# Performance work log

Measured on AMD Instinct MI355X. Metric: run time of the kernel, lower is better.

Reference implementation:

```python
import jax, jax.numpy as jnp
import numpy as np

B, L, H, S = 8, 2048, 8, 128


def setup_inputs() -> dict:
    key = jax.random.key(0)
    k1, k2, k3 = jax.random.split(key, 3)
    x = jax.random.normal(k1, (B, L, S), dtype=jnp.float32)
    W = jax.random.normal(k2, (L, H), dtype=jnp.float32)          # per-head Toeplitz logits, W[j, h] fills diagonal -j
    A = jax.random.normal(k3, (H * S, H * S), dtype=jnp.float32)  # bilinear form for stage-2 attention
    return {"x": x, "W": W, "A": A}


def reference(x, W, A):
    Bb, Ll, Ss = x.shape
    Hh = W.shape[1]
    HS = Hh * Ss
    # Stage 1: causal Toeplitz softmax attention per head.
    # Original fills diagonal -j of W_h with W[j, h], masks strictly-upper with -inf, softmaxes rows.
    d = jnp.arange(Ll)[:, None] - jnp.arange(Ll)[None, :]          # (L, L), i - j
    logits = jnp.where(d[..., None] >= 0,
                       W[jnp.clip(d, 0, Ll - 1)],                  # (L, L, H), W[i-j, h] on valid band
                       -jnp.inf)
    P = jax.nn.softmax(logits, axis=1)                             # softmax over key axis j
    attn = jnp.einsum('ijh,bjs->bihs', P, x).reshape(Bb, Ll, HS)   # heads concatenated
    X1 = jnp.concatenate([attn, x], axis=-1)                       # (B, L, (H+1)*S)
    # Stage 2: single-query bilinear attention from last token over previous tokens.
    q = X1[:, -1, :HS]                                             # (B, HS)
    keys = X1[:, :-1, :HS]                                         # (B, L-1, HS)
    scores = jnp.einsum('bd,de,ble->bl', q, A, keys)               # (B, L-1)
    w2 = jax.nn.softmax(scores, axis=-1)
    # values are the raw-x slice X1[:, :-1, HS:] == x[:, :-1, :]
    out = jnp.einsum('bl,bls->bs', w2, x[:, :-1, :])               # (B, S)
    return out
```

## Files before the change

### kernel.cpp

```cpp
#include <hip/hip_runtime.h>

#define L 2048
#define H 8
#define S 128
#define B 8
#define HS 1024

__global__ __launch_bounds__(512) void kA_prep_qpart(const float* __restrict__ W,
                                                     const float* __restrict__ x,
                                                     float* __restrict__ Eb,
                                                     float* __restrict__ Zb,
                                                     float* __restrict__ partial_q,
                                                     unsigned* __restrict__ counters) {
  const int b = blockIdx.x, jc = blockIdx.y;
  const int t = threadIdx.x;
  if (b == 0 && jc == 0 && t == 0) counters[0] = 0u;

  __shared__ float ew[128][H];
  __shared__ float part[16][H][S];
  __shared__ float tot[512];

  const int base = jc * 128;
  const int dhi = L - 1 - base;
#pragma unroll
  for (int k = 0; k < 2; ++k) {
    const int idx = t + k * 512;
    const int i = idx >> 3, h = idx & 7;
    ew[i][h] = expf(W[(size_t)(dhi - i) * H + h]);
  }

  if (jc < H) {
    const int h = jc;
    const int d0 = t * 4;
    float e[4];
    float run = 0.f;
#pragma unroll
    for (int k = 0; k < 4; ++k) {
      float v = expf(W[(size_t)(d0 + k) * H + h]);
      e[k] = v; run += v;
    }
    tot[t] = run;
    __syncthreads();
    for (int off = 1; off < 512; off <<= 1) {
      float v = (t >= off) ? tot[t - off] : 0.f;
      __syncthreads();
      tot[t] += v;
      __syncthreads();
    }
    float c = (t == 0) ? 0.f : tot[t - 1];
    const size_t ebase = (size_t)(b * H + h) * L;
#pragma unroll
    for (int k = 0; k < 4; ++k) {
      c += e[k];
      Eb[ebase + d0 + k] = e[k];
      Zb[ebase + d0 + k] = c;
    }
  }
  __syncthreads();

  const int s4 = t & 31;
  const int r = t >> 5;
  const float4* __restrict__ x4 = (const float4*)(x + (size_t)b * L * S);
  float4 acc[H];
#pragma unroll
  for (int h = 0; h < H; ++h) acc[h] = make_float4(0.f, 0.f, 0.f, 0.f);
#pragma unroll
  for (int k = 0; k < 8; ++k) {
    const int ll = k * 16 + r;
    const int l = base + ll;
    const float4 xv = x4[(size_t)l * 32 + s4];
#pragma unroll
    for (int h = 0; h < H; ++h) {
      const float w = ew[ll][h];
      acc[h].x += w * xv.x; acc[h].y += w * xv.y;
      acc[h].z += w * xv.z; acc[h].w += w * xv.w;
    }
  }
#pragma unroll
  for (int h = 0; h < H; ++h) {
    part[r][h][s4 * 4 + 0] = acc[h].x;
    part[r][h][s4 * 4 + 1] = acc[h].y;
    part[r][h][s4 * 4 + 2] = acc[h].z;
    part[r][h][s4 * 4 + 3] = acc[h].w;
  }
  __syncthreads();
#pragma unroll
  for (int k = 0; k < 2; ++k) {
    const int idx = t + k * 512;
    const int h = idx >> 7, s = idx & 127;
    float sm = 0.f;
#pragma unroll
    for (int rr = 0; rr < 16; ++rr) sm += part[rr][h][s];
    partial_q[((size_t)b * 16 + jc) * HS + idx] = sm;
  }
}

__global__ __launch_bounds__(512) void kB_v(const float* __restrict__ partial_q,
                                            const float* __restrict__ Zb,
                                            const float* __restrict__ A,
                                            float* __restrict__ partial_v) {
  const int ebase = blockIdx.x * 128;
  const int dc = blockIdx.y;
  const int dbase = dc * 64;
  const int t = threadIdx.x;
  __shared__ float ql[8][64];
  __shared__ float p2[4][8][128];
  const float invZ = 1.f / Zb[(size_t)(dc >> 1) * L + (L - 1)];
  {
    const int bb = t >> 6, dl = t & 63;
    const float* __restrict__ pq = partial_q + ((size_t)bb * 16) * HS + dbase + dl;
    float a0 = 0.f, a1 = 0.f, a2 = 0.f, a3 = 0.f;
#pragma unroll
    for (int j4 = 0; j4 < 16; j4 += 4) {
      a0 += pq[(size_t)(j4 + 0) * HS];
      a1 += pq[(size_t)(j4 + 1) * HS];
      a2 += pq[(size_t)(j4 + 2) * HS];
      a3 += pq[(size_t)(j4 + 3) * HS];
    }
    ql[bb][dl] = ((a0 + a1) + (a2 + a3)) * invZ;
  }
  __syncthreads();
  const int el = t & 127, dg = t >> 7;
  const int e = ebase + el;
  const float* __restrict__ Ab = A + (size_t)(dbase + dg * 16) * HS + e;
  float acc[8] = {0.f, 0.f, 0.f, 0.f, 0.f, 0.f, 0.f, 0.f};
#pragma unroll 4
  for (int dd = 0; dd < 16; ++dd) {
    const float a = Ab[(size_t)dd * HS];
    const int d = dg * 16 + dd;
    acc[0] += ql[0][d] * a;
    acc[1] += ql[1][d] * a;
    acc[2] += ql[2][d] * a;
    acc[3] += ql[3][d] * a;
    acc[4] += ql[4][d] * a;
    acc[5] += ql[5][d] * a;
    acc[6] += ql[6][d] * a;
    acc[7] += ql[7][d] * a;
  }
#pragma unroll
  for (int bb = 0; bb < 8; ++bb) p2[dg][bb][el] = acc[bb];
  __syncthreads();
#pragma unroll
  for (int k = 0; k < 2; ++k) {
    const int idx = t + k * 512;
    const int bb = idx >> 7, el2 = idx & 127;
    partial_v[((size_t)bb * 16 + dc) * HS + ebase + el2] =
        (p2[0][bb][el2] + p2[1][bb][el2]) + (p2[2][bb][el2] + p2[3][bb][el2]);
  }
}

__global__ __launch_bounds__(512) void kC_u(const float* __restrict__ x,
                                            const float* __restrict__ partial_v,
                                            float* __restrict__ u_pad) {
  const int b = blockIdx.x, jc = blockIdx.y;
  const int t = threadIdx.x;
  __shared__ float vs[HS];
  __shared__ float up[4][H][128];
#pragma unroll
  for (int k = 0; k < 2; ++k) {
    const int i = t + k * 512;
    float a0 = 0.f, a1 = 0.f, a2 = 0.f, a3 = 0.f;
#pragma unroll
    for (int dcc = 0; dcc < 16; dcc += 4) {
      a0 += partial_v[((size_t)b * 16 + dcc + 0) * HS + i];
      a1 += partial_v[((size_t)b * 16 + dcc + 1) * HS + i];
      a2 += partial_v[((size_t)b * 16 + dcc + 2) * HS + i];
      a3 += partial_v[((size_t)b * 16 + dcc + 3) * HS + i];
    }
    vs[i] = (a0 + a1) + (a2 + a3);
  }
  __syncthreads();
  const int jl = t & 127, sq = t >> 7;
  const int j = jc * 128 + jl;
  const float4* __restrict__ xr = (const float4*)(x + ((size_t)b * L + j) * S) + sq * 8;
  float4 xv[8];
#pragma unroll
  for (int i = 0; i < 8; ++i) xv[i] = xr[i];
  float acc[H];
#pragma unroll
  for (int h = 0; h < H; ++h) {
    const float4* __restrict__ vv = (const float4*)(vs + h * S + sq * 32);
    float a = 0.f;
#pragma unroll
    for (int i = 0; i < 8; ++i) {
      const float4 w = vv[i];
      a += xv[i].x * w.x + xv[i].y * w.y + xv[i].z * w.z + xv[i].w * w.w;
    }
    acc[h] = a;
  }
#pragma unroll
  for (int h = 0; h < H; ++h) up[sq][h][jl] = acc[h];
  __syncthreads();
#pragma unroll
  for (int k = 0; k < 2; ++k) {
    const int idx = t + k * 512;
    const int h = idx >> 7, j2 = idx & 127;
    const float sv = (up[0][h][j2] + up[1][h][j2]) + (up[2][h][j2] + up[3][h][j2]);
    const size_t rowbase = (size_t)(b * H + h) * (2 * L);
    u_pad[rowbase + jc * 128 + j2] = 0.f;
    u_pad[rowbase + L + jc * 128 + j2] = sv;
  }
}

__global__ __launch_bounds__(512) void kD_conv(const float* __restrict__ u_pad,
                                               const float* __restrict__ Eb,
                                               const float* __restrict__ Zb,
                                               float* __restrict__ partial_s) {
  const int b = blockIdx.x;
  const int rr = blockIdx.y;
  int lt = 0, c = 0;
  while (c + (lt / 2 + 1) <= rr) { c += lt / 2 + 1; ++lt; }
  const int dtt = rr - c;
  const int l0 = lt * 128;
  const int t = threadIdx.x;
  const int tsub = t & 31;
  const int h = (t >> 5) & 7;
  const int dh = t >> 8;
  const int dbase = dtt * 256 + dh * 128;
  const int Lb = l0 + tsub * 4;
  const float* __restrict__ ur = u_pad + (size_t)(b * H + h) * (2 * L) + L;
  const float4* __restrict__ Eh4 = (const float4*)(Eb + (size_t)(b * H + h) * L);
  float acc0 = 0.f, acc1 = 0.f, acc2 = 0.f, acc3 = 0.f;
  float4 lo = *(const float4*)(ur + Lb - dbase - 4);
  float4 hi = *(const float4*)(ur + Lb - dbase);
#pragma unroll 4
  for (int dd = 0; dd < 128; dd += 4) {
    const int d0 = dbase + dd;
    float4 ev  = Eh4[d0 >> 2];
    float4 nlo = *(const float4*)(ur + Lb - d0 - 8);
    acc0 += ev.x * hi.x; acc1 += ev.x * hi.y; acc2 += ev.x * hi.z; acc3 += ev.x * hi.w;
    acc0 += ev.y * lo.w; acc1 += ev.y * hi.x; acc2 += ev.y * hi.y; acc3 += ev.y * hi.z;
    acc0 += ev.z * lo.z; acc1 += ev.z * lo.w; acc2 += ev.z * hi.x; acc3 += ev.z * hi.y;
    acc0 += ev.w * lo.y; acc1 += ev.w * lo.z; acc2 += ev.w * lo.w; acc3 += ev.w * hi.x;
    hi = lo; lo = nlo;
  }
  __shared__ float sred[2][H][128];
  const float4 zv = *(const float4*)&Zb[(size_t)(b * H + h) * L + Lb];
  sred[dh][h][tsub * 4 + 0] = acc0 / zv.x;
  sred[dh][h][tsub * 4 + 1] = acc1 / zv.y;
  sred[dh][h][tsub * 4 + 2] = acc2 / zv.z;
  sred[dh][h][tsub * 4 + 3] = acc3 / zv.w;
  __syncthreads();
  if (t < 128) {
    float sc = 0.f;
#pragma unroll
    for (int hh = 0; hh < H; ++hh) sc += sred[0][hh][t] + sred[1][hh][t];
    partial_s[((size_t)b * 8 + dtt) * L + l0 + t] = sc;
  }
}

__global__ __launch_bounds__(512) void kF_out(const float* __restrict__ x,
                                              const float* __restrict__ partial_s,
                                              float* __restrict__ partial,
                                              unsigned* __restrict__ counters,
                                              float* __restrict__ out) {
  const int b = blockIdx.x, c = blockIdx.y;
  const int t = threadIdx.x;
  __shared__ float ep[L];
  __shared__ float red[512];
  __shared__ float part[16][S];

  const int l0 = t * 4;
  const int ltq = t >> 6;
  float sc[4] = {0.f, 0.f, 0.f, 0.f};
  for (int dtt = 0; dtt <= ltq; ++dtt) {
    const float4 a = *(const float4*)(partial_s + ((size_t)b * 8 + dtt) * L + l0);
    sc[0] += a.x; sc[1] += a.y; sc[2] += a.z; sc[3] += a.w;
  }
  if (t == 511) sc[3] = -3.4e38f;
  float mx = fmaxf(fmaxf(sc[0], sc[1]), fmaxf(sc[2], sc[3]));
  red[t] = mx;
  __syncthreads();
  for (int off = 256; off > 0; off >>= 1) {
    if (t < off) red[t] = fmaxf(red[t], red[t + off]);
    __syncthreads();
  }
  mx = red[0];
  __syncthreads();
  float e[4];
  float sm = 0.f;
#pragma unroll
  for (int k = 0; k < 4; ++k) {
    e[k] = (l0 + k < L - 1) ? expf(sc[k] - mx) : 0.f;
    sm += e[k];
  }
  red[t] = sm;
  __syncthreads();
  for (int off = 256; off > 0; off >>= 1) {
    if (t < off) red[t] += red[t + off];
    __syncthreads();
  }
  const float inv = 1.f / red[0];
#pragma unroll
  for (int k = 0; k < 4; ++k) ep[l0 + k] = e[k] * inv;
  __syncthreads();

  const int s4 = t & 31;
  const int r = t >> 5;
  const int base = c * 128;
  const float4* __restrict__ x4 = (const float4*)(x + (size_t)b * L * S);
  float4 acc = make_float4(0.f, 0.f, 0.f, 0.f);
#pragma unroll
  for (int k = 0; k < 8; ++k) {
    const int l = base + k * 16 + r;
    const float w = ep[l];
    const float4 xv = x4[(size_t)l * 32 + s4];
    acc.x += w * xv.x; acc.y += w * xv.y; acc.z += w * xv.z; acc.w += w * xv.w;
  }
  part[r][s4 * 4 + 0] = acc.x;
  part[r][s4 * 4 + 1] = acc.y;
  part[r][s4 * 4 + 2] = acc.z;
  part[r][s4 * 4 + 3] = acc.w;
  __syncthreads();
  if (t < S) {
    float smv = 0.f;
#pragma unroll
    for (int rr = 0; rr < 16; ++rr) smv += part[rr][t];
    partial[((size_t)b * 16 + c) * S + t] = smv;
  }
  __threadfence();
  __syncthreads();
  __shared__ unsigned lastFlag;
  if (t == 0)
    lastFlag = (atomicAdd(&counters[0], 1u) == (unsigned)(B * 16 - 1)) ? 1u : 0u;
  __syncthreads();
  if (lastFlag) {
#pragma unroll
    for (int k = 0; k < 2; ++k) {
      const int idx = t + k * 512;
      const int b2 = idx >> 7, s = idx & 127;
      float a = 0.f;
#pragma unroll 4
      for (int cc = 0; cc < 16; ++cc) a += partial[((size_t)b2 * 16 + cc) * S + s];
      out[b2 * S + s] = a;
    }
  }
}

extern "C" void kernel_launch(void* const* d_in, const int* in_sizes, int n_in,
                              void* d_out, int out_size, void* d_ws, size_t ws_size,
                              hipStream_t stream) {
  const float* x = (const float*)d_in[0];
  const float* W = (const float*)d_in[1];
  const float* A = (const float*)d_in[2];
  float* out = (float*)d_out;

  float* ws        = (float*)d_ws;
  float* Eb        = ws;
  float* Zb        = Eb + (size_t)B * H * L;
  float* partial_q = Zb + (size_t)B * H * L;
  float* partial_v = partial_q + (size_t)B * 16 * HS;
  float* u_pad     = partial_v + (size_t)B * 16 * HS;
  float* partial_s = u_pad + (size_t)B * H * 2 * L;
  float* partial   = partial_s + (size_t)B * 8 * L;
  unsigned* counters = (unsigned*)(partial + (size_t)B * 16 * S);

  kA_prep_qpart<<<dim3(B, 16), 512, 0, stream>>>(W, x, Eb, Zb, partial_q, counters);
  kB_v         <<<dim3(8, 16), 512, 0, stream>>>(partial_q, Zb, A, partial_v);
  kC_u         <<<dim3(B, 16), 512, 0, stream>>>(x, partial_v, u_pad);
  kD_conv      <<<dim3(B, 72), 512, 0, stream>>>(u_pad, Eb, Zb, partial_s);
  kF_out       <<<dim3(B, 16), 512, 0, stream>>>(x, partial_s, partial, counters, out);
}
```

Before: 55.93 us.

## Fuse convolution and output kernels with per-batch last-block softmax reduction

Merges the convolution kernel and the softmax/output kernel into one launch. Each block now loops over all causal diagonal chunks for its row tile instead of splitting chunks across 72 blocks per batch, and writes full scores directly. The last block per batch, found with a per-batch atomic counter, does the softmax and the full weighted sum over x. This removes a kernel launch and the partial-score buffer, but drops parallelism: the grid shrinks from 72 to 16 blocks per batch with uneven per-block work, and one block per batch does the whole output reduction serially.

Result: slower. 62.76 us (+12.2%).

```diff
diff --git a/kernel.cpp b/kernel.cpp
--- a/kernel.cpp
+++ b/kernel.cpp
@@ -14,7 +14,7 @@
                                                      unsigned* __restrict__ counters) {
   const int b = blockIdx.x, jc = blockIdx.y;
   const int t = threadIdx.x;
-  if (b == 0 && jc == 0 && t == 0) counters[0] = 0u;
+  if (b == 0 && jc == 0 && t < 8) counters[t] = 0u;
 
   __shared__ float ew[128][H];
   __shared__ float part[16][H][S];
@@ -202,39 +202,45 @@
   }
 }
 
-__global__ __launch_bounds__(512) void kD_conv(const float* __restrict__ u_pad,
+__global__ __launch_bounds__(512) void kDF_out(const float* __restrict__ x,
+                                               const float* __restrict__ u_pad,
                                                const float* __restrict__ Eb,
                                                const float* __restrict__ Zb,
-                                               float* __restrict__ partial_s) {
-  const int b = blockIdx.x;
-  const int rr = blockIdx.y;
-  int lt = 0, c = 0;
-  while (c + (lt / 2 + 1) <= rr) { c += lt / 2 + 1; ++lt; }
-  const int dtt = rr - c;
-  const int l0 = lt * 128;
+                                               float* __restrict__ scores,
+                                               unsigned* __restrict__ counters,
+                                               float* __restrict__ out) {
+  const int b = blockIdx.x, lt = blockIdx.y;
   const int t = threadIdx.x;
   const int tsub = t & 31;
   const int h = (t >> 5) & 7;
   const int dh = t >> 8;
-  const int dbase = dtt * 256 + dh * 128;
+  const int l0 = lt * 128;
   const int Lb = l0 + tsub * 4;
+
+  __shared__ float sred[2][H][128];
+  __shared__ float ep[L];
+  __shared__ float red[512];
+  __shared__ float part[16][S];
+
   const float* __restrict__ ur = u_pad + (size_t)(b * H + h) * (2 * L) + L;
   const float4* __restrict__ Eh4 = (const float4*)(Eb + (size_t)(b * H + h) * L);
   float acc0 = 0.f, acc1 = 0.f, acc2 = 0.f, acc3 = 0.f;
-  float4 lo = *(const float4*)(ur + Lb - dbase - 4);
-  float4 hi = *(const float4*)(ur + Lb - dbase);
+  for (int chunk = dh; chunk <= lt; chunk += 2) {
+    const int dbase = chunk * 128;
+    float4 lo = *(const float4*)(ur + Lb - dbase - 4);
+    float4 hi = *(const float4*)(ur + Lb - dbase);
 #pragma unroll 4
-  for (int dd = 0; dd < 128; dd += 4) {
-    const int d0 = dbase + dd;
-    float4 ev  = Eh4[d0 >> 2];
-    float4 nlo = *(const float4*)(ur + Lb - d0 - 8);
-    acc0 += ev.x * hi.x; acc1 += ev.x * hi.y; acc2 += ev.x * hi.z; acc3 += ev.x * hi.w;
-    acc0 += ev.y * lo.w; acc1 += ev.y * hi.x; acc2 += ev.y * hi.y; acc3 += ev.y * hi.z;
-    acc0 += ev.z * lo.z; acc1 += ev.z * lo.w; acc2 += ev.z * hi.x; acc3 += ev.z * hi.y;
-    acc0 += ev.w * lo.y; acc1 += ev.w * lo.z; acc2 += ev.w * lo.w; acc3 += ev.w * hi.x;
-    hi = lo; lo = nlo;
-  }
-  __shared__ float sred[2][H][128];
+    for (int dd = 0; dd < 128; dd += 4) {
+      const int d0 = dbase + dd;
+      float4 ev  = Eh4[d0 >> 2];
+      float4 nlo = *(const float4*)(ur + Lb - d0 - 8);
+      acc0 += ev.x * hi.x; acc1 += ev.x * hi.y; acc2 += ev.x * hi.z; acc3 += ev.x * hi.w;
+      acc0 += ev.y * lo.w; acc1 += ev.y * hi.x; acc2 += ev.y * hi.y; acc3 += ev.y * hi.z;
+      acc0 += ev.z * lo.z; acc1 += ev.z * lo.w; acc2 += ev.z * hi.x; acc3 += ev.z * hi.y;
+      acc0 += ev.w * lo.y; acc1 += ev.w * lo.z; acc2 += ev.w * lo.w; acc3 += ev.w * hi.x;
+      hi = lo; lo = nlo;
+    }
+  }
   const float4 zv = *(const float4*)&Zb[(size_t)(b * H + h) * L + Lb];
   sred[dh][h][tsub * 4 + 0] = acc0 / zv.x;
   sred[dh][h][tsub * 4 + 1] = acc1 / zv.y;
@@ -242,33 +248,24 @@
   sred[dh][h][tsub * 4 + 3] = acc3 / zv.w;
   __syncthreads();
   if (t < 128) {
+    const int l = l0 + t;
     float sc = 0.f;
 #pragma unroll
     for (int hh = 0; hh < H; ++hh) sc += sred[0][hh][t] + sred[1][hh][t];
-    partial_s[((size_t)b * 8 + dtt) * L + l0 + t] = sc;
-  }
-}
-
-__global__ __launch_bounds__(512) void kF_out(const float* __restrict__ x,
-                                              const float* __restrict__ partial_s,
-                                              float* __restrict__ partial,
-                                              unsigned* __restrict__ counters,
-                                              float* __restrict__ out) {
-  const int b = blockIdx.x, c = blockIdx.y;
-  const int t = threadIdx.x;
-  __shared__ float ep[L];
-  __shared__ float red[512];
-  __shared__ float part[16][S];
-
-  const int l0 = t * 4;
-  const int ltq = t >> 6;
-  float sc[4] = {0.f, 0.f, 0.f, 0.f};
-  for (int dtt = 0; dtt <= ltq; ++dtt) {
-    const float4 a = *(const float4*)(partial_s + ((size_t)b * 8 + dtt) * L + l0);
-    sc[0] += a.x; sc[1] += a.y; sc[2] += a.z; sc[3] += a.w;
-  }
-  if (t == 511) sc[3] = -3.4e38f;
-  float mx = fmaxf(fmaxf(sc[0], sc[1]), fmaxf(sc[2], sc[3]));
+    scores[(size_t)b * L + l] = (l == L - 1) ? -3.4e38f : sc;
+  }
+
+  __threadfence();
+  __syncthreads();
+  __shared__ unsigned lastFlag;
+  if (t == 0)
+    lastFlag = (atomicAdd(&counters[b], 1u) == 15u) ? 1u : 0u;
+  __syncthreads();
+  if (!lastFlag) return;
+
+  const int l4 = t * 4;
+  const float4 sv4 = *(const float4*)&scores[(size_t)b * L + l4];
+  float mx = fmaxf(fmaxf(sv4.x, sv4.y), fmaxf(sv4.z, sv4.w));
   red[t] = mx;
   __syncthreads();
   for (int off = 256; off > 0; off >>= 1) {
@@ -277,32 +274,27 @@
   }
   mx = red[0];
   __syncthreads();
-  float e[4];
-  float sm = 0.f;
-#pragma unroll
-  for (int k = 0; k < 4; ++k) {
-    e[k] = (l0 + k < L - 1) ? expf(sc[k] - mx) : 0.f;
-    sm += e[k];
-  }
-  red[t] = sm;
+  float e0 = expf(sv4.x - mx), e1 = expf(sv4.y - mx);
+  float e2 = expf(sv4.z - mx), e3 = expf(sv4.w - mx);
+  red[t] = (e0 + e1) + (e2 + e3);
   __syncthreads();
   for (int off = 256; off > 0; off >>= 1) {
     if (t < off) red[t] += red[t + off];
     __syncthreads();
   }
   const float inv = 1.f / red[0];
-#pragma unroll
-  for (int k = 0; k < 4; ++k) ep[l0 + k] = e[k] * inv;
+  ep[l4 + 0] = e0 * inv;
+  ep[l4 + 1] = e1 * inv;
+  ep[l4 + 2] = e2 * inv;
+  ep[l4 + 3] = e3 * inv;
   __syncthreads();
 
   const int s4 = t & 31;
   const int r = t >> 5;
-  const int base = c * 128;
   const float4* __restrict__ x4 = (const float4*)(x + (size_t)b * L * S);
   float4 acc = make_float4(0.f, 0.f, 0.f, 0.f);
-#pragma unroll
-  for (int k = 0; k < 8; ++k) {
-    const int l = base + k * 16 + r;
+  for (int k = 0; k < 128; ++k) {
+    const int l = k * 16 + r;
     const float w = ep[l];
     const float4 xv = x4[(size_t)l * 32 + s4];
     acc.x += w * xv.x; acc.y += w * xv.y; acc.z += w * xv.z; acc.w += w * xv.w;
@@ -316,24 +308,7 @@
     float smv = 0.f;
 #pragma unroll
     for (int rr = 0; rr < 16; ++rr) smv += part[rr][t];
-    partial[((size_t)b * 16 + c) * S + t] = smv;
-  }
-  __threadfence();
-  __syncthreads();
-  __shared__ unsigned lastFlag;
-  if (t == 0)
-    lastFlag = (atomicAdd(&counters[0], 1u) == (unsigned)(B * 16 - 1)) ? 1u : 0u;
-  __syncthreads();
-  if (lastFlag) {
-#pragma unroll
-    for (int k = 0; k < 2; ++k) {
-      const int idx = t + k * 512;
-      const int b2 = idx >> 7, s = idx & 127;
-      float a = 0.f;
-#pragma unroll 4
-      for (int cc = 0; cc < 16; ++cc) a += partial[((size_t)b2 * 16 + cc) * S + s];
-      out[b2 * S + s] = a;
-    }
+    out[b * S + t] = smv;
   }
 }
 
@@ -351,13 +326,11 @@
   float* partial_q = Zb + (size_t)B * H * L;
   float* partial_v = partial_q + (size_t)B * 16 * HS;
   float* u_pad     = partial_v + (size_t)B * 16 * HS;
-  float* partial_s = u_pad + (size_t)B * H * 2 * L;
-  float* partial   = partial_s + (size_t)B * 8 * L;
-  unsigned* counters = (unsigned*)(partial + (size_t)B * 16 * S);
+  float* scores    = u_pad + (size_t)B * H * 2 * L;
+  unsigned* counters = (unsigned*)(scores + (size_t)B * L);
 
   kA_prep_qpart<<<dim3(B, 16), 512, 0, stream>>>(W, x, Eb, Zb, partial_q, counters);
   kB_v         <<<dim3(8, 16), 512, 0, stream>>>(partial_q, Zb, A, partial_v);
   kC_u         <<<dim3(B, 16), 512, 0, stream>>>(x, partial_v, u_pad);
-  kD_conv      <<<dim3(B, 72), 512, 0, stream>>>(u_pad, Eb, Zb, partial_s);
-  kF_out       <<<dim3(B, 16), 512, 0, stream>>>(x, partial_s, partial, counters, out);
-}
+  kDF_out      <<<dim3(B, 16), 512, 0, stream>>>(x, u_pad, Eb, Zb, scores, counters, out);
+}
```
